# Performance work log

Hardware: AMD Instinct MI355X
Metric: run time of the kernel (lower is better)

## Reference

```python
import jax, jax.numpy as jnp
import numpy as np

B, N, IN_F = 32, 512, 128
H, DK, DV, OUT_F = 8, 16, 16, 128
TOPK = 16
NEG = -1e9
SCALE = 1.0 / (DK ** 0.5)


def setup_inputs() -> dict:
    key = jax.random.key(0)
    ks = jax.random.split(key, 8)
    s_in = (1.0 / IN_F) ** 0.5   # torch Linear default init scale (uniform approximated by scaled normal)
    s_hid = (1.0 / (H * DV)) ** 0.5
    return {
        "x": jax.random.normal(ks[0], (B, N, IN_F), jnp.float32),
        "mask": jax.random.randint(ks[1], (B, N, N), 0, 2, jnp.int32),
        "Wq": jax.random.normal(ks[2], (IN_F, H * DK), jnp.float32) * s_in,
        "bq": jnp.zeros((H * DK,), jnp.float32),
        "Wk": jax.random.normal(ks[3], (IN_F, H * DK), jnp.float32) * s_in,
        "bk": jnp.zeros((H * DK,), jnp.float32),
        "Wv": jax.random.normal(ks[4], (IN_F, H * DV), jnp.float32) * s_in,
        "bv": jnp.zeros((H * DV,), jnp.float32),
        "Wout": jax.random.normal(ks[5], (H * DV, OUT_F), jnp.float32) * s_hid,
        "bout": jnp.zeros((OUT_F,), jnp.float32),
    }


def _attention(x, mask, Wq, bq, Wk, bk, Wv, bv, Wout, bout):
    b, n, _ = x.shape
    # vkq_activation_fn = relu applied to projections, then heads split: [B,H,N,D]
    q = jax.nn.relu(x @ Wq + bq).reshape(b, n, H, DK).transpose(0, 2, 1, 3)
    k = jax.nn.relu(x @ Wk + bk).reshape(b, n, H, DK).transpose(0, 2, 1, 3)
    v = jax.nn.relu(x @ Wv + bv).reshape(b, n, H, DV).transpose(0, 2, 1, 3)
    att_logits = jnp.einsum("bhqd,bhkd->bhqk", q, k) * SCALE  # [B,H,N,N]
    adj = mask[:, None, :, :] != 0  # broadcast over heads
    masked = jnp.where(adj, att_logits, NEG)
    # top-k sparsification along last dim, exact scatter of selected indices
    _, idx = jax.lax.top_k(masked, TOPK)  # [B,H,N,TOPK]
    flat = masked.reshape(-1, n)
    rows = jnp.arange(flat.shape[0])[:, None]
    smask = jnp.zeros(flat.shape, bool).at[rows, idx.reshape(-1, TOPK)].set(True)
    att = jnp.where(smask.reshape(masked.shape), masked, NEG)
    probs = jax.nn.softmax(att, axis=-1)
    out = jnp.einsum("bhqk,bhkd->bhqd", probs, v) + v  # residual add with v
    out = out.transpose(0, 2, 1, 3).reshape(b, n, H * DV)
    out = jax.nn.relu(out @ Wout + bout)  # activation_fn = relu
    return out, att_logits


def reference(x, mask, Wq, bq, Wk, bk, Wv, bv, Wout, bout):
    return _attention(x, mask, Wq, bq, Wk, bk, Wv, bv, Wout, bout)
```

## Files before the change

### kernel.cpp

```cpp
#include <hip/hip_runtime.h>
#include <math.h>

#define NB    32
#define SEQ   512
#define INF_  128
#define NH    8
#define HD    16
#define NEGV  (-1e9f)
#define SCALE_ 0.25f

template<int CTRL>
__device__ __forceinline__ float dpp_max_step(float x){
  int xi = __float_as_int(x);
  int yi = __builtin_amdgcn_update_dpp(xi, xi, CTRL, 0xF, 0xF, false);
  return fmaxf(x, __int_as_float(yi));
}
__device__ __forceinline__ float wave_max_all(float x){
  x = dpp_max_step<0x111>(x);
  x = dpp_max_step<0x112>(x);
  x = dpp_max_step<0x114>(x);
  x = dpp_max_step<0x118>(x);
  x = dpp_max_step<0x142>(x);
  x = dpp_max_step<0x143>(x);
  return __int_as_float(__builtin_amdgcn_readlane(__float_as_int(x), 63));
}
template<int CTRL, int ROWMASK>
__device__ __forceinline__ int dpp_add_step(int x){
  int y = __builtin_amdgcn_update_dpp(0, x, CTRL, ROWMASK, 0xF, false);
  return x + y;
}
__device__ __forceinline__ int wave_iscan(int x){
  x = dpp_add_step<0x111, 0xF>(x);
  x = dpp_add_step<0x112, 0xF>(x);
  x = dpp_add_step<0x114, 0xF>(x);
  x = dpp_add_step<0x118, 0xF>(x);
  x = dpp_add_step<0x142, 0xa>(x);
  x = dpp_add_step<0x143, 0xc>(x);
  return x;
}
template<int CTRL>
__device__ __forceinline__ void dpp_max2_step(unsigned &hi, unsigned &lo){
  unsigned oh = (unsigned)__builtin_amdgcn_update_dpp((int)hi, (int)hi, CTRL, 0xF, 0xF, false);
  unsigned ol = (unsigned)__builtin_amdgcn_update_dpp((int)lo, (int)lo, CTRL, 0xF, 0xF, false);
  bool gt = (oh > hi) | ((oh == hi) & (ol > lo));
  hi = gt ? oh : hi;
  lo = gt ? ol : lo;
}

#define CSW(a,b) { float hi_ = fmaxf(a,b); float lo_ = fminf(a,b); a = hi_; b = lo_; }

__global__ __launch_bounds__(256) void qkv_kernel(
    const float* __restrict__ x,
    const float* __restrict__ Wq, const float* __restrict__ bq,
    const float* __restrict__ Wk, const float* __restrict__ bk,
    const float* __restrict__ Wv, const float* __restrict__ bv,
    float* __restrict__ qo, float* __restrict__ ko, float* __restrict__ vo)
{
  __shared__ float xs[32*128];
  const int tid = threadIdx.x;
  const size_t row0 = (size_t)blockIdx.x * 32;
  const float4* xg = (const float4*)(x + row0*INF_);
  float4* xs4 = (float4*)xs;
  for (int t = tid; t < 1024; t += 256) xs4[t] = xg[t];
  __syncthreads();

  const int wave = tid >> 6, lane = tid & 63;
  const int r0 = wave * 8;
  float aq0[8], aq1[8], ak0[8], ak1[8], av0[8], av1[8];
  #pragma unroll
  for (int r=0;r<8;r++){ aq0[r]=aq1[r]=ak0[r]=ak1[r]=av0[r]=av1[r]=0.f; }

  for (int kb = 0; kb < 128; kb += 4){
    float4 xv[8];
    #pragma unroll
    for (int r=0;r<8;r++) xv[r] = *(const float4*)&xs[(r0+r)*INF_ + kb];
    #pragma unroll
    for (int kk=0;kk<4;kk++){
      const int krow = (kb+kk)*INF_;
      float wq0 = Wq[krow + lane], wq1 = Wq[krow + lane + 64];
      float wk0 = Wk[krow + lane], wk1 = Wk[krow + lane + 64];
      float wv0 = Wv[krow + lane], wv1 = Wv[krow + lane + 64];
      #pragma unroll
      for (int r=0;r<8;r++){
        float xr = (kk==0)? xv[r].x : (kk==1)? xv[r].y : (kk==2)? xv[r].z : xv[r].w;
        aq0[r] = fmaf(xr, wq0, aq0[r]); aq1[r] = fmaf(xr, wq1, aq1[r]);
        ak0[r] = fmaf(xr, wk0, ak0[r]); ak1[r] = fmaf(xr, wk1, ak1[r]);
        av0[r] = fmaf(xr, wv0, av0[r]); av1[r] = fmaf(xr, wv1, av1[r]);
      }
    }
  }
  float bq0 = bq[lane], bq1 = bq[lane+64];
  float bk0_ = bk[lane], bk1_ = bk[lane+64];
  float bv0_ = bv[lane], bv1_ = bv[lane+64];
  #pragma unroll
  for (int r=0;r<8;r++){
    size_t o = (row0 + r0 + r)*INF_;
    qo[o + lane]      = fmaxf(aq0[r] + bq0, 0.f);
    qo[o + lane + 64] = fmaxf(aq1[r] + bq1, 0.f);
    ko[o + lane]      = fmaxf(ak0[r] + bk0_, 0.f);
    ko[o + lane + 64] = fmaxf(ak1[r] + bk1_, 0.f);
    vo[o + lane]      = fmaxf(av0[r] + bv0_, 0.f);
    vo[o + lane + 64] = fmaxf(av1[r] + bv1_, 0.f);
  }
}

__global__ __launch_bounds__(512, 2) void attn_kernel(
    const float* __restrict__ qg, const float* __restrict__ kg, const float* __restrict__ vg,
    const int* __restrict__ mask, float* __restrict__ logits_out, float* __restrict__ att_out)
{
  __shared__ float K_lds[512*20];
  __shared__ float V_lds[512*16];
  __shared__ float Q_lds[256*16];
  __shared__ float pv_s[8*16];
  __shared__ int   pi_s[8*16];

  const int tid  = threadIdx.x;
  const int bh   = blockIdx.x >> 1;
  const int split= blockIdx.x & 1;
  const int b    = bh >> 3, h = bh & 7;
  const int n0   = split * 256;
  const size_t base_bh = ((size_t)b * SEQ) * INF_ + (size_t)h * HD;

  for (int t = tid; t < 2048; t += 512){
    int row = t >> 2, c = t & 3;
    float4 k4 = *(const float4*)(kg + base_bh + (size_t)row*INF_ + c*4);
    *(float4*)&K_lds[row*20 + c*4] = k4;
    float4 v4 = *(const float4*)(vg + base_bh + (size_t)row*INF_ + c*4);
    *(float4*)&V_lds[row*16 + c*4] = v4;
  }
  for (int t = tid; t < 1024; t += 512){
    int row = t >> 2, c = t & 3;
    float4 q4 = *(const float4*)(qg + base_bh + (size_t)(n0+row)*INF_ + c*4);
    *(float4*)&Q_lds[row*16 + c*4] = q4;
  }
  __syncthreads();

  const int wave = tid >> 6, lane = tid & 63;
  const int wavebase = wave * 16;

  #pragma unroll 1
  for (int g = 0; g < 8; ++g){
    const int nl = wave*32 + g*4;
    const int n  = n0 + nl;

    int mreg[4][8];
    const int* mrow = mask + ((size_t)b*SEQ + n)*SEQ + lane;
    #pragma unroll
    for (int r=0;r<4;r++)
      #pragma unroll
      for (int kk=0;kk<8;kk++)
        mreg[r][kk] = mrow[(size_t)r*SEQ + kk*64];

    float4 qv[4][4];
    #pragma unroll
    for (int r=0;r<4;r++){
      const float4* qp = (const float4*)&Q_lds[(nl+r)*16];
      #pragma unroll
      for (int c=0;c<4;c++) qv[r][c] = qp[c];
    }

    float acc[4][8];
    #pragma unroll
    for (int r=0;r<4;r++)
      #pragma unroll
      for (int kk=0;kk<8;kk++) acc[r][kk] = 0.f;

    #pragma unroll
    for (int kk=0;kk<8;kk++){
      const float4* Kp = (const float4*)&K_lds[(lane + kk*64)*20];
      float4 k0 = Kp[0], k1 = Kp[1], k2 = Kp[2], k3 = Kp[3];
      #pragma unroll
      for (int r=0;r<4;r++){
        float a = acc[r][kk];
        a = fmaf(qv[r][0].x, k0.x, a); a = fmaf(qv[r][0].y, k0.y, a);
        a = fmaf(qv[r][0].z, k0.z, a); a = fmaf(qv[r][0].w, k0.w, a);
        a = fmaf(qv[r][1].x, k1.x, a); a = fmaf(qv[r][1].y, k1.y, a);
        a = fmaf(qv[r][1].z, k1.z, a); a = fmaf(qv[r][1].w, k1.w, a);
        a = fmaf(qv[r][2].x, k2.x, a); a = fmaf(qv[r][2].y, k2.y, a);
        a = fmaf(qv[r][2].z, k2.z, a); a = fmaf(qv[r][2].w, k2.w, a);
        a = fmaf(qv[r][3].x, k3.x, a); a = fmaf(qv[r][3].y, k3.y, a);
        a = fmaf(qv[r][3].z, k3.z, a); a = fmaf(qv[r][3].w, k3.w, a);
        acc[r][kk] = a;
      }
    }

    float* lbase = logits_out + (((size_t)(b*NH + h)*SEQ + n)*SEQ) + lane;

    #pragma unroll 1
    for (int r=0;r<4;r++){
      const int n_r = n + r;
      float mv[8];
      #pragma unroll
      for (int kk=0;kk<8;kk++){
        float a  = (r==0)? acc[0][kk] : (r==1)? acc[1][kk] : (r==2)? acc[2][kk] : acc[3][kk];
        int   mm = (r==0)? mreg[0][kk]: (r==1)? mreg[1][kk]: (r==2)? mreg[2][kk]: mreg[3][kk];
        float sv = a * SCALE_;
        lbase[(size_t)r*SEQ + kk*64] = sv;
        mv[kk] = (mm != 0) ? sv : NEGV;
      }

      float s0=mv[0], s1=mv[1], s2=mv[2], s3=mv[3], s4=mv[4], s5=mv[5], s6=mv[6], s7=mv[7];
      CSW(s0,s1) CSW(s2,s3) CSW(s4,s5) CSW(s6,s7)
      CSW(s0,s2) CSW(s1,s3) CSW(s4,s6) CSW(s5,s7)
      CSW(s1,s2) CSW(s5,s6)
      CSW(s0,s4) CSW(s1,s5) CSW(s2,s6) CSW(s3,s7)
      CSW(s2,s4) CSW(s3,s5)
      CSW(s1,s2) CSW(s3,s4) CSW(s5,s6)

      float cur = s0;
      float M = 0.f, T = 0.f;
      for (int it=0; it<16; ++it){
        float m = wave_max_all(cur);
        if (it == 0) M = m;
        T = m;
        if (cur == m){
          s0=s1; s1=s2; s2=s3; s3=s4; s4=s5; s5=s6; s6=s7;
          s7 = -__builtin_inff();
          cur = s0;
        }
      }

      int cnt = 0, selb = 0;
      #pragma unroll
      for (int kk=0;kk<8;kk++){
        bool s_ = (mv[kk] >= T);
        cnt += s_ ? 1 : 0;
        selb |= s_ ? (1<<kk) : 0;
      }
      int incl  = wave_iscan(cnt);
      int total = __builtin_amdgcn_readlane(incl, 63);
      int pos   = wavebase + (incl - cnt);

      if (total == 16){
        #pragma unroll
        for (int kk=0;kk<8;kk++){
          if (selb & (1<<kk)){
            pv_s[pos] = mv[kk];
            pi_s[pos] = lane + (kk<<6);
            ++pos;
          }
        }
      } else {
        unsigned kh[8], kl[8];
        #pragma unroll
        for (int kk=0;kk<8;kk++){
          unsigned u = (unsigned)__float_as_int(mv[kk]);
          u = u ^ ((u & 0x80000000u) ? 0xFFFFFFFFu : 0x80000000u);
          kh[kk] = u;
          kl[kk] = (unsigned)(511 - (lane + (kk<<6)));
        }
        for (int it=0; it<16; ++it){
          unsigned bh_ = kh[0], bl_ = kl[0];
          #pragma unroll
          for (int kk=1;kk<8;kk++){
            bool g_ = (kh[kk] > bh_) | ((kh[kk]==bh_) & (kl[kk] > bl_));
            bh_ = g_ ? kh[kk] : bh_;
            bl_ = g_ ? kl[kk] : bl_;
          }
          dpp_max2_step<0x111>(bh_, bl_);
          dpp_max2_step<0x112>(bh_, bl_);
          dpp_max2_step<0x114>(bh_, bl_);
          dpp_max2_step<0x118>(bh_, bl_);
          dpp_max2_step<0x142>(bh_, bl_);
          dpp_max2_step<0x143>(bh_, bl_);
          unsigned mh = (unsigned)__builtin_amdgcn_readlane((int)bh_, 63);
          unsigned ml = (unsigned)__builtin_amdgcn_readlane((int)bl_, 63);
          int widx = 511 - (int)ml;
          #pragma unroll
          for (int kk=0;kk<8;kk++){
            if (kh[kk]==mh && kl[kk]==ml){
              pv_s[wavebase + it] = mv[kk];
              pi_s[wavebase + it] = widx;
              kh[kk] = 0u; kl[kk] = 0u;
            }
          }
        }
      }

      asm volatile("s_waitcnt lgkmcnt(0)" ::: "memory");
      __builtin_amdgcn_sched_barrier(0);
      const int rep = lane >> 4;
      const int d   = lane & 15;
      float o = 0.f, sp = 0.f;
      #pragma unroll
      for (int j=0;j<4;j++){
        const int i = wavebase + rep*4 + j;
        float vv = pv_s[i];
        int  idx = pi_s[i];
        float p = __expf(vv - M);
        o  = fmaf(p, V_lds[idx*16 + d], o);
        sp += p;
      }
      o  += __shfl_xor(o, 16);
      o  += __shfl_xor(o, 32);
      sp += __shfl_xor(sp, 16);
      sp += __shfl_xor(sp, 32);
      float res = o / sp + V_lds[n_r*16 + d];
      if (lane < 16)
        att_out[((size_t)b*SEQ + n_r)*INF_ + (size_t)h*HD + d] = res;
    }
  }
}

__global__ __launch_bounds__(256) void out_kernel(
    const float* __restrict__ a, const float* __restrict__ W, const float* __restrict__ bias,
    float* __restrict__ out)
{
  __shared__ float xs[32*128];
  const int tid = threadIdx.x;
  const size_t row0 = (size_t)blockIdx.x * 32;
  const float4* ag = (const float4*)(a + row0*INF_);
  float4* xs4 = (float4*)xs;
  for (int t = tid; t < 1024; t += 256) xs4[t] = ag[t];
  __syncthreads();

  const int wave = tid >> 6, lane = tid & 63;
  const int r0 = wave * 8;
  float a0[8], a1[8];
  #pragma unroll
  for (int r=0;r<8;r++){ a0[r]=a1[r]=0.f; }

  for (int kb = 0; kb < 128; kb += 4){
    float4 xv[8];
    #pragma unroll
    for (int r=0;r<8;r++) xv[r] = *(const float4*)&xs[(r0+r)*INF_ + kb];
    #pragma unroll
    for (int kk=0;kk<4;kk++){
      const int krow = (kb+kk)*INF_;
      float w0 = W[krow + lane], w1 = W[krow + lane + 64];
      #pragma unroll
      for (int r=0;r<8;r++){
        float xr = (kk==0)? xv[r].x : (kk==1)? xv[r].y : (kk==2)? xv[r].z : xv[r].w;
        a0[r] = fmaf(xr, w0, a0[r]);
        a1[r] = fmaf(xr, w1, a1[r]);
      }
    }
  }
  float b0 = bias[lane], b1 = bias[lane+64];
  #pragma unroll
  for (int r=0;r<8;r++){
    size_t o = (row0 + r0 + r)*INF_;
    out[o + lane]      = fmaxf(a0[r] + b0, 0.f);
    out[o + lane + 64] = fmaxf(a1[r] + b1, 0.f);
  }
}

extern "C" void kernel_launch(void* const* d_in, const int* in_sizes, int n_in,
                              void* d_out, int out_size, void* d_ws, size_t ws_size,
                              hipStream_t stream)
{
  const float* x    = (const float*)d_in[0];
  const int*   mask = (const int*)  d_in[1];
  const float* Wq   = (const float*)d_in[2];
  const float* bq   = (const float*)d_in[3];
  const float* Wk   = (const float*)d_in[4];
  const float* bk   = (const float*)d_in[5];
  const float* Wv   = (const float*)d_in[6];
  const float* bv   = (const float*)d_in[7];
  const float* Wout = (const float*)d_in[8];
  const float* bout = (const float*)d_in[9];

  float* out_f  = (float*)d_out;
  float* logits = out_f + (size_t)NB*SEQ*INF_;

  float* qws = (float*)d_ws;
  float* kws = qws + (size_t)NB*SEQ*INF_;
  float* vws = kws + (size_t)NB*SEQ*INF_;
  float* aws = vws + (size_t)NB*SEQ*INF_;

  qkv_kernel<<<512, 256, 0, stream>>>(x, Wq,bq, Wk,bk, Wv,bv, qws, kws, vws);
  attn_kernel<<<512, 512, 0, stream>>>(qws, kws, vws, mask, logits, aws);
  out_kernel<<<512, 256, 0, stream>>>(aws, Wout, bout, out_f);
}
```

Measured before the change: 561.8 us.

## Interleave top-k threshold search across row pairs and raise attention occupancy

The attention kernel now processes query rows in pairs, interleaving two independent wave-wide max reductions in a fully unrolled, branchless threshold loop to hide DPP latency. It drops the Q shared-memory staging in favour of direct global loads, which frees LDS. It packs mask values into bitmasks to cut register use, and raises the launch-bounds occupancy target from 2 to 4 blocks. The higher occupancy target may force register spills, since the unrolled paired loop holds more live values.

```diff
diff --git a/kernel.cpp b/kernel.cpp
--- a/kernel.cpp
+++ b/kernel.cpp
@@ -104,13 +104,12 @@
   }
 }
 
-__global__ __launch_bounds__(512, 2) void attn_kernel(
+__global__ __launch_bounds__(512, 4) void attn_kernel(
     const float* __restrict__ qg, const float* __restrict__ kg, const float* __restrict__ vg,
     const int* __restrict__ mask, float* __restrict__ logits_out, float* __restrict__ att_out)
 {
   __shared__ float K_lds[512*20];
   __shared__ float V_lds[512*16];
-  __shared__ float Q_lds[256*16];
   __shared__ float pv_s[8*16];
   __shared__ int   pi_s[8*16];
 
@@ -128,11 +127,6 @@
     float4 v4 = *(const float4*)(vg + base_bh + (size_t)row*INF_ + c*4);
     *(float4*)&V_lds[row*16 + c*4] = v4;
   }
-  for (int t = tid; t < 1024; t += 512){
-    int row = t >> 2, c = t & 3;
-    float4 q4 = *(const float4*)(qg + base_bh + (size_t)(n0+row)*INF_ + c*4);
-    *(float4*)&Q_lds[row*16 + c*4] = q4;
-  }
   __syncthreads();
 
   const int wave = tid >> 6, lane = tid & 63;
@@ -154,7 +148,7 @@
     float4 qv[4][4];
     #pragma unroll
     for (int r=0;r<4;r++){
-      const float4* qp = (const float4*)&Q_lds[(nl+r)*16];
+      const float4* qp = (const float4*)(qg + base_bh + (size_t)(n+r)*INF_);
       #pragma unroll
       for (int c=0;c<4;c++) qv[r][c] = qp[c];
     }
@@ -184,120 +178,154 @@
       }
     }
 
+    int mbits[4];
+    #pragma unroll
+    for (int r=0;r<4;r++){
+      int mb = 0;
+      #pragma unroll
+      for (int kk=0;kk<8;kk++) mb |= (mreg[r][kk] != 0) ? (1<<kk) : 0;
+      mbits[r] = mb;
+    }
+
     float* lbase = logits_out + (((size_t)(b*NH + h)*SEQ + n)*SEQ) + lane;
 
-    #pragma unroll 1
-    for (int r=0;r<4;r++){
-      const int n_r = n + r;
-      float mv[8];
+    #pragma unroll
+    for (int pr=0; pr<2; ++pr){
+      const int rA = 2*pr, rB = 2*pr + 1;
+
       #pragma unroll
       for (int kk=0;kk<8;kk++){
-        float a  = (r==0)? acc[0][kk] : (r==1)? acc[1][kk] : (r==2)? acc[2][kk] : acc[3][kk];
-        int   mm = (r==0)? mreg[0][kk]: (r==1)? mreg[1][kk]: (r==2)? mreg[2][kk]: mreg[3][kk];
-        float sv = a * SCALE_;
-        lbase[(size_t)r*SEQ + kk*64] = sv;
-        mv[kk] = (mm != 0) ? sv : NEGV;
-      }
-
-      float s0=mv[0], s1=mv[1], s2=mv[2], s3=mv[3], s4=mv[4], s5=mv[5], s6=mv[6], s7=mv[7];
-      CSW(s0,s1) CSW(s2,s3) CSW(s4,s5) CSW(s6,s7)
-      CSW(s0,s2) CSW(s1,s3) CSW(s4,s6) CSW(s5,s7)
-      CSW(s1,s2) CSW(s5,s6)
-      CSW(s0,s4) CSW(s1,s5) CSW(s2,s6) CSW(s3,s7)
-      CSW(s2,s4) CSW(s3,s5)
-      CSW(s1,s2) CSW(s3,s4) CSW(s5,s6)
-
-      float cur = s0;
-      float M = 0.f, T = 0.f;
+        float svA = acc[rA][kk] * SCALE_;
+        float svB = acc[rB][kk] * SCALE_;
+        lbase[(size_t)rA*SEQ + kk*64] = svA;
+        lbase[(size_t)rB*SEQ + kk*64] = svB;
+        acc[rA][kk] = (mbits[rA] & (1<<kk)) ? svA : NEGV;
+        acc[rB][kk] = (mbits[rB] & (1<<kk)) ? svB : NEGV;
+      }
+
+      float a0=acc[rA][0], a1=acc[rA][1], a2=acc[rA][2], a3=acc[rA][3],
+            a4=acc[rA][4], a5=acc[rA][5], a6=acc[rA][6], a7=acc[rA][7];
+      float b0=acc[rB][0], b1=acc[rB][1], b2=acc[rB][2], b3=acc[rB][3],
+            b4=acc[rB][4], b5=acc[rB][5], b6=acc[rB][6], b7=acc[rB][7];
+      CSW(a0,a1) CSW(a2,a3) CSW(a4,a5) CSW(a6,a7)
+      CSW(b0,b1) CSW(b2,b3) CSW(b4,b5) CSW(b6,b7)
+      CSW(a0,a2) CSW(a1,a3) CSW(a4,a6) CSW(a5,a7)
+      CSW(b0,b2) CSW(b1,b3) CSW(b4,b6) CSW(b5,b7)
+      CSW(a1,a2) CSW(a5,a6)
+      CSW(b1,b2) CSW(b5,b6)
+      CSW(a0,a4) CSW(a1,a5) CSW(a2,a6) CSW(a3,a7)
+      CSW(b0,b4) CSW(b1,b5) CSW(b2,b6) CSW(b3,b7)
+      CSW(a2,a4) CSW(a3,a5)
+      CSW(b2,b4) CSW(b3,b5)
+      CSW(a1,a2) CSW(a3,a4) CSW(a5,a6)
+      CSW(b1,b2) CSW(b3,b4) CSW(b5,b6)
+
+      float curA = a0, curB = b0;
+      float MA = 0.f, TA = 0.f, MB = 0.f, TB = 0.f;
+      #pragma unroll
       for (int it=0; it<16; ++it){
-        float m = wave_max_all(cur);
-        if (it == 0) M = m;
-        T = m;
-        if (cur == m){
-          s0=s1; s1=s2; s2=s3; s3=s4; s4=s5; s5=s6; s6=s7;
-          s7 = -__builtin_inff();
-          cur = s0;
-        }
-      }
-
-      int cnt = 0, selb = 0;
-      #pragma unroll
-      for (int kk=0;kk<8;kk++){
-        bool s_ = (mv[kk] >= T);
-        cnt += s_ ? 1 : 0;
-        selb |= s_ ? (1<<kk) : 0;
-      }
-      int incl  = wave_iscan(cnt);
-      int total = __builtin_amdgcn_readlane(incl, 63);
-      int pos   = wavebase + (incl - cnt);
-
-      if (total == 16){
+        float mA = wave_max_all(curA);
+        float mB = wave_max_all(curB);
+        if (it == 0){ MA = mA; MB = mB; }
+        TA = mA; TB = mB;
+        bool cA = (curA == mA);
+        a0 = cA ? a1 : a0; a1 = cA ? a2 : a1; a2 = cA ? a3 : a2; a3 = cA ? a4 : a3;
+        a4 = cA ? a5 : a4; a5 = cA ? a6 : a5; a6 = cA ? a7 : a6;
+        a7 = cA ? -__builtin_inff() : a7;
+        curA = a0;
+        bool cB = (curB == mB);
+        b0 = cB ? b1 : b0; b1 = cB ? b2 : b1; b2 = cB ? b3 : b2; b3 = cB ? b4 : b3;
+        b4 = cB ? b5 : b4; b5 = cB ? b6 : b5; b6 = cB ? b7 : b6;
+        b7 = cB ? -__builtin_inff() : b7;
+        curB = b0;
+      }
+
+      #pragma unroll
+      for (int rr=0; rr<2; ++rr){
+        const int r   = 2*pr + rr;
+        const int n_r = n + r;
+        const float T = rr ? TB : TA;
+        const float M = rr ? MB : MA;
+
+        int cnt = 0, selb = 0;
         #pragma unroll
         for (int kk=0;kk<8;kk++){
-          if (selb & (1<<kk)){
-            pv_s[pos] = mv[kk];
-            pi_s[pos] = lane + (kk<<6);
-            ++pos;
-          }
+          bool s_ = (acc[r][kk] >= T);
+          cnt += s_ ? 1 : 0;
+          selb |= s_ ? (1<<kk) : 0;
         }
-      } else {
-        unsigned kh[8], kl[8];
-        #pragma unroll
-        for (int kk=0;kk<8;kk++){
-          unsigned u = (unsigned)__float_as_int(mv[kk]);
-          u = u ^ ((u & 0x80000000u) ? 0xFFFFFFFFu : 0x80000000u);
-          kh[kk] = u;
-          kl[kk] = (unsigned)(511 - (lane + (kk<<6)));
-        }
-        for (int it=0; it<16; ++it){
-          unsigned bh_ = kh[0], bl_ = kl[0];
-          #pragma unroll
-          for (int kk=1;kk<8;kk++){
-            bool g_ = (kh[kk] > bh_) | ((kh[kk]==bh_) & (kl[kk] > bl_));
-            bh_ = g_ ? kh[kk] : bh_;
-            bl_ = g_ ? kl[kk] : bl_;
-          }
-          dpp_max2_step<0x111>(bh_, bl_);
-          dpp_max2_step<0x112>(bh_, bl_);
-          dpp_max2_step<0x114>(bh_, bl_);
-          dpp_max2_step<0x118>(bh_, bl_);
-          dpp_max2_step<0x142>(bh_, bl_);
-          dpp_max2_step<0x143>(bh_, bl_);
-          unsigned mh = (unsigned)__builtin_amdgcn_readlane((int)bh_, 63);
-          unsigned ml = (unsigned)__builtin_amdgcn_readlane((int)bl_, 63);
-          int widx = 511 - (int)ml;
+        int incl  = wave_iscan(cnt);
+        int total = __builtin_amdgcn_readlane(incl, 63);
+        int pos   = wavebase + (incl - cnt);
+
+        if (total == 16){
           #pragma unroll
           for (int kk=0;kk<8;kk++){
-            if (kh[kk]==mh && kl[kk]==ml){
-              pv_s[wavebase + it] = mv[kk];
-              pi_s[wavebase + it] = widx;
-              kh[kk] = 0u; kl[kk] = 0u;
+            if (selb & (1<<kk)){
+              pv_s[pos] = acc[r][kk];
+              pi_s[pos] = lane + (kk<<6);
+              ++pos;
+            }
+          }
+        } else {
+          unsigned kh[8], kl[8];
+          #pragma unroll
+          for (int kk=0;kk<8;kk++){
+            unsigned u = (unsigned)__float_as_int(acc[r][kk]);
+            u = u ^ ((u & 0x80000000u) ? 0xFFFFFFFFu : 0x80000000u);
+            kh[kk] = u;
+            kl[kk] = (unsigned)(511 - (lane + (kk<<6)));
+          }
+          for (int it=0; it<16; ++it){
+            unsigned bh_ = kh[0], bl_ = kl[0];
+            #pragma unroll
+            for (int kk=1;kk<8;kk++){
+              bool g_ = (kh[kk] > bh_) | ((kh[kk]==bh_) & (kl[kk] > bl_));
+              bh_ = g_ ? kh[kk] : bh_;
+              bl_ = g_ ? kl[kk] : bl_;
+            }
+            dpp_max2_step<0x111>(bh_, bl_);
+            dpp_max2_step<0x112>(bh_, bl_);
+            dpp_max2_step<0x114>(bh_, bl_);
+            dpp_max2_step<0x118>(bh_, bl_);
+            dpp_max2_step<0x142>(bh_, bl_);
+            dpp_max2_step<0x143>(bh_, bl_);
+            unsigned mh = (unsigned)__builtin_amdgcn_readlane((int)bh_, 63);
+            unsigned ml = (unsigned)__builtin_amdgcn_readlane((int)bl_, 63);
+            int widx = 511 - (int)ml;
+            #pragma unroll
+            for (int kk=0;kk<8;kk++){
+              if (kh[kk]==mh && kl[kk]==ml){
+                pv_s[wavebase + it] = acc[r][kk];
+                pi_s[wavebase + it] = widx;
+                kh[kk] = 0u; kl[kk] = 0u;
+              }
             }
           }
         }
-      }
-
-      asm volatile("s_waitcnt lgkmcnt(0)" ::: "memory");
-      __builtin_amdgcn_sched_barrier(0);
-      const int rep = lane >> 4;
-      const int d   = lane & 15;
-      float o = 0.f, sp = 0.f;
-      #pragma unroll
-      for (int j=0;j<4;j++){
-        const int i = wavebase + rep*4 + j;
-        float vv = pv_s[i];
-        int  idx = pi_s[i];
-        float p = __expf(vv - M);
-        o  = fmaf(p, V_lds[idx*16 + d], o);
-        sp += p;
-      }
-      o  += __shfl_xor(o, 16);
-      o  += __shfl_xor(o, 32);
-      sp += __shfl_xor(sp, 16);
-      sp += __shfl_xor(sp, 32);
-      float res = o / sp + V_lds[n_r*16 + d];
-      if (lane < 16)
-        att_out[((size_t)b*SEQ + n_r)*INF_ + (size_t)h*HD + d] = res;
+
+        asm volatile("s_waitcnt lgkmcnt(0)" ::: "memory");
+        __builtin_amdgcn_sched_barrier(0);
+        const int rep = lane >> 4;
+        const int d   = lane & 15;
+        float o = 0.f, sp = 0.f;
+        #pragma unroll
+        for (int j=0;j<4;j++){
+          const int i = wavebase + rep*4 + j;
+          float vv = pv_s[i];
+          int  idx = pi_s[i];
+          float p = __expf(vv - M);
+          o  = fmaf(p, V_lds[idx*16 + d], o);
+          sp += p;
+        }
+        o  += __shfl_xor(o, 16);
+        o  += __shfl_xor(o, 32);
+        sp += __shfl_xor(sp, 16);
+        sp += __shfl_xor(sp, 32);
+        float res = o / sp + V_lds[n_r*16 + d];
+        if (lane < 16)
+          att_out[((size_t)b*SEQ + n_r)*INF_ + (size_t)h*HD + d] = res;
+      }
     }
   }
 }
```

New measurement: 854.8 us. 1.52x slower.
